# Optimization experiments

Measured on AMD Instinct MI355X. Metric: run time of the kernel, lower is better.

Reference implementation:

```python
import jax, jax.numpy as jnp
import numpy as np

H = 32        # num_attention_heads
KVH = 8       # num_key_value_heads
D = 64        # attention_head_size
WIN = 256     # attention_window_size (left/right)
ROPE_BASE = 10000.0


def setup_inputs() -> dict:
    key = jax.random.key(0)
    k1, k2, k3 = jax.random.split(key, 3)
    B, S = 2, 2048
    return {
        "query_states": jax.random.normal(k1, (B, S, H * D), dtype=jnp.float32),
        "key_states": jax.random.normal(k2, (B, S, KVH * D), dtype=jnp.float32),
        "value_states": jax.random.normal(k3, (B, S, KVH * D), dtype=jnp.float32),
    }


def _rope_cos_sin(seq_len, dtype):
    inv_freq = 1.0 / (ROPE_BASE ** (jnp.arange(0, D, 2, dtype=jnp.float32) / D))  # [D/2]
    pos = jnp.arange(seq_len, dtype=jnp.float32)
    freqs = pos[:, None] * inv_freq[None, :]          # [S, D/2]
    emb = jnp.concatenate([freqs, freqs], axis=-1)    # [S, D]
    return jnp.cos(emb).astype(dtype), jnp.sin(emb).astype(dtype)


def _rotate_half(x):
    x1, x2 = x[..., : D // 2], x[..., D // 2 :]
    return jnp.concatenate([-x2, x1], axis=-1)


def reference(query_states, key_states, value_states):
    B, S, _ = query_states.shape
    n_rep = H // KVH

    q = query_states.reshape(B, S, H, D).transpose(0, 2, 1, 3)        # [B,H,S,D]
    k = key_states.reshape(B, S, KVH, D).transpose(0, 2, 1, 3)        # [B,KVH,S,D]
    v = value_states.reshape(B, S, KVH, D).transpose(0, 2, 1, 3)

    # repeat_kv: [B,KVH,S,D] -> [B,H,S,D]
    k = jnp.repeat(k, n_rep, axis=1)
    v = jnp.repeat(v, n_rep, axis=1)

    cos, sin = _rope_cos_sin(S, q.dtype)   # [S,D]
    cos = cos[None, None]                  # [1,1,S,D]
    sin = sin[None, None]
    q = q * cos + _rotate_half(q) * sin
    k = k * cos + _rotate_half(k) * sin

    scale = 1.0 / jnp.sqrt(jnp.asarray(D, dtype=q.dtype))
    scores = jnp.einsum("bhqd,bhkd->bhqk", q, k) * scale              # [B,H,S,S]

    i = jnp.arange(S)[:, None]
    j = jnp.arange(S)[None, :]
    allowed = (j >= i - WIN) & (j <= i)                               # [S,S]
    scores = jnp.where(allowed[None, None], scores, jnp.finfo(scores.dtype).min)

    probs = jax.nn.softmax(scores, axis=-1)
    out = jnp.einsum("bhqk,bhkd->bhqd", probs, v)                     # [B,H,S,D]
    return out.transpose(0, 2, 1, 3).reshape(B, S, H * D)
```

## Files before the change

kernel.cpp:

```cpp
#include <hip/hip_runtime.h>
#include <math.h>

#define NH   32
#define NKVH 8
#define HD   64
#define WIN  256
#define BB   2
#define SS   2048

typedef short short8 __attribute__((ext_vector_type(8)));
typedef float f32x4  __attribute__((ext_vector_type(4)));

__device__ __forceinline__ ushort f2bf(float x) {
    union { float f; unsigned u; } v; v.f = x;
    unsigned u = v.u + 0x7FFF + ((v.u >> 16) & 1);
    return (ushort)(u >> 16);
}

__device__ __forceinline__ int cvtpk_bf16(float lo, float hi) {
    int r;
    asm("v_cvt_pk_bf16_f32 %0, %1, %2" : "=v"(r) : "v"(lo), "v"(hi));
    return r;
}

__device__ __forceinline__ int swz(int L) { return L ^ (((L >> 7) & 7) << 4); }

__device__ __forceinline__ void stage16(const void* g, void* l) {
    __builtin_amdgcn_global_load_lds(
        (const __attribute__((address_space(1))) unsigned int*)g,
        (__attribute__((address_space(3))) unsigned int*)l, 16, 0, 0);
}

__global__ __launch_bounds__(256) void prep_kv(const float* __restrict__ K,
                                               const float* __restrict__ V,
                                               ushort* __restrict__ Kr,
                                               ushort* __restrict__ Vt) {
    __shared__ __align__(16) ushort ldsK[2048];
    __shared__ __align__(16) ushort ldsV[2048];
    const int bidx = blockIdx.x;
    const int sblk = bidx & 63;
    const int s0   = sblk * 32;
    const int kvh  = (bidx >> 6) & 7;
    const int b    = bidx >> 9;
    const int tid  = threadIdx.x;

    {
        const int key = tid >> 3, dg = tid & 7;
        const int s   = s0 + key;
        const float* krow = K + (size_t)(b * SS + s) * (NKVH * HD) + kvh * HD + dg * 8;
        float x[8];
        *(float4*)(x)     = *(const float4*)(krow);
        *(float4*)(x + 4) = *(const float4*)(krow + 4);
        float inv = __powf(10000.f, -(float)((dg & 3) * 8) * (1.f / 32.f));
        const float ratio = 0.74989420933f;
        ushort out[8];
#pragma unroll
        for (int j = 0; j < 8; ++j) {
            float partner = __shfl(x[j], (tid & 63) ^ 4, 64);
            float sn, cs;
            __sincosf((float)s * inv, &sn, &cs);
            out[j] = f2bf(x[j] * cs + ((dg < 4) ? -partner : partner) * sn);
            inv *= ratio;
        }
        *(short8*)((char*)ldsK + swz(key * 128 + dg * 16)) = *(short8*)out;
    }
    {
        const int kp = tid & 15, dq = tid >> 4;
        const float* v0 = V + (size_t)(b * SS + s0 + 2 * kp) * (NKVH * HD) + kvh * HD + dq * 4;
        float4 a = *(const float4*)v0;
        float4 c = *(const float4*)(v0 + NKVH * HD);
#pragma unroll
        for (int j = 0; j < 4; ++j) {
            int d = dq * 4 + j;
            unsigned w = (unsigned)f2bf(((const float*)&a)[j])
                       | ((unsigned)f2bf(((const float*)&c)[j]) << 16);
            *(unsigned*)((char*)ldsV + swz(d * 64 + kp * 4)) = w;
        }
    }
    __syncthreads();
    char* kc = (char*)(Kr + (size_t)(b * NKVH + kvh) * SS * HD) + (size_t)sblk * 4096;
    char* vc = (char*)(Vt + (size_t)(b * NKVH + kvh) * HD * SS) + (size_t)sblk * 4096;
    *(short8*)(kc + tid * 16) = *(short8*)((char*)ldsK + tid * 16);
    *(short8*)(vc + tid * 16) = *(short8*)((char*)ldsV + tid * 16);
}

__global__ __launch_bounds__(256, 4) void attn_mfma(const float* __restrict__ Q,
                                                    const ushort* __restrict__ Kr,
                                                    const ushort* __restrict__ Vt,
                                                    float* __restrict__ O) {
    __shared__ __align__(16) ushort ldsK[2][2][2048];
    __shared__ __align__(16) ushort ldsV[2][2][2048];
    const int wv = threadIdx.x >> 6, lane = threadIdx.x & 63;
    const int lo16 = lane & 15, quad = lane >> 4;
    const int bidx = (blockIdx.x & 7) * 128 + (blockIdx.x >> 3);
    const int qblk = bidx & 63;
    const int kvh  = (bidx >> 6) & 7;
    const int b    = bidx >> 9;
    const int h    = kvh * 4 + wv;
    const int q0   = qblk * 32;

    float invf[8];
#pragma unroll
    for (int j = 0; j < 8; ++j)
        invf[j] = __powf(10000.f, -(float)(quad * 8 + j) * (1.f / 32.f));

    short8 aq[2][2];
#pragma unroll
    for (int t = 0; t < 2; ++t) {
        int qi = q0 + t * 16 + lo16;
        const float* qrow = Q + (size_t)(b * SS + qi) * (NH * HD) + h * HD;
        float lo[8], hi[8];
        *(float4*)(lo)     = *(const float4*)(qrow + quad * 8);
        *(float4*)(lo + 4) = *(const float4*)(qrow + quad * 8 + 4);
        *(float4*)(hi)     = *(const float4*)(qrow + 32 + quad * 8);
        *(float4*)(hi + 4) = *(const float4*)(qrow + 32 + quad * 8 + 4);
#pragma unroll
        for (int j = 0; j < 8; ++j) {
            float sn, cs;
            __sincosf((float)qi * invf[j], &sn, &cs);
            aq[t][0][j] = (short)f2bf((lo[j] * cs - hi[j] * sn) * 0.125f);
            aq[t][1][j] = (short)f2bf((hi[j] * cs + lo[j] * sn) * 0.125f);
        }
    }

    const char* kbase = (const char*)(Kr + (size_t)(b * NKVH + kvh) * SS * HD);
    const char* vbase = (const char*)(Vt + (size_t)(b * NKVH + kvh) * HD * SS);

    f32x4 acc[2][4];
#pragma unroll
    for (int t = 0; t < 2; ++t)
#pragma unroll
        for (int i = 0; i < 4; ++i) acc[t][i] = (f32x4){0.f, 0.f, 0.f, 0.f};
    float psum[2] = {0.f, 0.f};

    const int idxAB = (lo16 + ((quad & 1) << 5)) << 2;
    const int idxCD = idxAB + 64;
    const bool hiq  = quad >= 2;

    int klo = q0 - WIN; if (klo < 0) klo = 0;
    const int c0  = klo >> 5;
    const int cnt = (q0 >> 5) - c0 + 1;
    const int npairs = (cnt + 1) >> 1;

    auto stagepair = [&](int pidx, int buf) {
        int ca = c0 + 2 * pidx, cb = ca + 1;
        if (ca > SS / 32 - 1) ca = SS / 32 - 1;
        if (cb > SS / 32 - 1) cb = SS / 32 - 1;
        stage16(kbase + (size_t)ca * 4096 + wv * 1024 + lane * 16,
                (char*)&ldsK[buf][0][0] + wv * 1024);
        stage16(vbase + (size_t)ca * 4096 + wv * 1024 + lane * 16,
                (char*)&ldsV[buf][0][0] + wv * 1024);
        stage16(kbase + (size_t)cb * 4096 + wv * 1024 + lane * 16,
                (char*)&ldsK[buf][1][0] + wv * 1024);
        stage16(vbase + (size_t)cb * 4096 + wv * 1024 + lane * 16,
                (char*)&ldsV[buf][1][0] + wv * 1024);
    };

    auto compute = [&](int kb, const char* kl, const char* vl) {
        short8 k0 = *(const short8*)(kl + swz(lo16 * 128 + quad * 16));
        short8 k1 = *(const short8*)(kl + swz(lo16 * 128 + 64 + quad * 16));
        short8 k2 = *(const short8*)(kl + swz((lo16 + 16) * 128 + quad * 16));
        short8 k3 = *(const short8*)(kl + swz((lo16 + 16) * 128 + 64 + quad * 16));

        const f32x4 z = {0.f, 0.f, 0.f, 0.f};
        __builtin_amdgcn_s_setprio(1);
        f32x4 s00 = __builtin_amdgcn_mfma_f32_16x16x32_bf16(k0, aq[0][0], z,   0, 0, 0);
        s00       = __builtin_amdgcn_mfma_f32_16x16x32_bf16(k1, aq[0][1], s00, 0, 0, 0);
        f32x4 s01 = __builtin_amdgcn_mfma_f32_16x16x32_bf16(k2, aq[0][0], z,   0, 0, 0);
        s01       = __builtin_amdgcn_mfma_f32_16x16x32_bf16(k3, aq[0][1], s01, 0, 0, 0);
        f32x4 s10 = __builtin_amdgcn_mfma_f32_16x16x32_bf16(k0, aq[1][0], z,   0, 0, 0);
        s10       = __builtin_amdgcn_mfma_f32_16x16x32_bf16(k1, aq[1][1], s10, 0, 0, 0);
        f32x4 s11 = __builtin_amdgcn_mfma_f32_16x16x32_bf16(k2, aq[1][0], z,   0, 0, 0);
        s11       = __builtin_amdgcn_mfma_f32_16x16x32_bf16(k3, aq[1][1], s11, 0, 0, 0);
        __builtin_amdgcn_s_setprio(0);

        short8 ap[2];
#pragma unroll
        for (int t = 0; t < 2; ++t) {
            const f32x4 sa = t ? s10 : s00;
            const f32x4 sb = t ? s11 : s01;
            const int qtmin = q0 + t * 16;
            const int myq   = qtmin + lo16;
            float p[8];
            if ((kb + 31 > qtmin) || (kb < qtmin + 15 - WIN)) {
#pragma unroll
                for (int r = 0; r < 4; ++r) {
                    int key0 = kb + quad * 4 + r;
                    int key1 = key0 + 16;
                    p[r]     = (key0 <= myq && key0 >= myq - WIN) ? __expf(sa[r]) : 0.f;
                    p[4 + r] = (key1 <= myq && key1 >= myq - WIN) ? __expf(sb[r]) : 0.f;
                }
            } else {
#pragma unroll
                for (int r = 0; r < 4; ++r) { p[r] = __expf(sa[r]); p[4 + r] = __expf(sb[r]); }
            }
            psum[t] += ((p[0] + p[1]) + (p[2] + p[3])) + ((p[4] + p[5]) + (p[6] + p[7]));

            int w0 = cvtpk_bf16(p[0], p[1]);
            int w1 = cvtpk_bf16(p[2], p[3]);
            int w2 = cvtpk_bf16(p[4], p[5]);
            int w3 = cvtpk_bf16(p[6], p[7]);
            int a0 = __builtin_amdgcn_ds_bpermute(idxAB, w0);
            int a2 = __builtin_amdgcn_ds_bpermute(idxAB, w2);
            int b1 = __builtin_amdgcn_ds_bpermute(idxAB, w1);
            int b3 = __builtin_amdgcn_ds_bpermute(idxAB, w3);
            int cc0 = __builtin_amdgcn_ds_bpermute(idxCD, w0);
            int cc2 = __builtin_amdgcn_ds_bpermute(idxCD, w2);
            int d1 = __builtin_amdgcn_ds_bpermute(idxCD, w1);
            int d3 = __builtin_amdgcn_ds_bpermute(idxCD, w3);
            union { int i[4]; short8 s; } u;
            u.i[0] = hiq ? a2  : a0;
            u.i[1] = hiq ? b3  : b1;
            u.i[2] = hiq ? cc2 : cc0;
            u.i[3] = hiq ? d3  : d1;
            ap[t] = u.s;
        }

        short8 vf[4];
#pragma unroll
        for (int i = 0; i < 4; ++i)
            vf[i] = *(const short8*)(vl + swz((i * 16 + lo16) * 64 + quad * 16));

        __builtin_amdgcn_s_setprio(1);
#pragma unroll
        for (int i = 0; i < 4; ++i)
            acc[0][i] = __builtin_amdgcn_mfma_f32_16x16x32_bf16(ap[0], vf[i], acc[0][i], 0, 0, 0);
#pragma unroll
        for (int i = 0; i < 4; ++i)
            acc[1][i] = __builtin_amdgcn_mfma_f32_16x16x32_bf16(ap[1], vf[i], acc[1][i], 0, 0, 0);
        __builtin_amdgcn_s_setprio(0);
    };

    stagepair(0, 0);

    int nb = 0;
    for (int p = 0; p < npairs; ++p, nb ^= 1) {
        stagepair(p + 1, nb ^ 1);
        asm volatile("s_waitcnt vmcnt(4)" ::: "memory");
        __builtin_amdgcn_s_barrier();
        __builtin_amdgcn_sched_barrier(0);
        compute(klo + 2 * p * 32, (const char*)&ldsK[nb][0][0], (const char*)&ldsV[nb][0][0]);
        if (2 * p + 1 < cnt)
            compute(klo + (2 * p + 1) * 32, (const char*)&ldsK[nb][1][0], (const char*)&ldsV[nb][1][0]);
        __builtin_amdgcn_sched_barrier(0);
        __builtin_amdgcn_s_barrier();
    }

#pragma unroll
    for (int t = 0; t < 2; ++t) {
        float ps = psum[t];
        ps += __shfl_xor(ps, 16, 64);
        ps += __shfl_xor(ps, 32, 64);
#pragma unroll
        for (int r = 0; r < 4; ++r) {
            float invr = 1.f / __shfl(ps, quad * 4 + r, 16);
            int qr = q0 + t * 16 + quad * 4 + r;
            size_t orow = ((size_t)(b * SS + qr) * NH + h) * HD;
            O[orow + 0 * 16 + lo16] = acc[t][0][r] * invr;
            O[orow + 1 * 16 + lo16] = acc[t][1][r] * invr;
            O[orow + 2 * 16 + lo16] = acc[t][2][r] * invr;
            O[orow + 3 * 16 + lo16] = acc[t][3][r] * invr;
        }
    }
}

__device__ __forceinline__ float wave_sum(float x) {
#pragma unroll
    for (int off = 32; off > 0; off >>= 1) x += __shfl_xor(x, off, 64);
    return x;
}

__global__ __launch_bounds__(256) void attn_scalar(const float* __restrict__ Q,
                                                   const float* __restrict__ K,
                                                   const float* __restrict__ V,
                                                   float* __restrict__ O) {
    int wave = blockIdx.x * 4 + (threadIdx.x >> 6);
    int lane = threadIdx.x & 63;
    int q  = wave % SS;
    int bh = wave / SS;
    int h  = bh % NH;
    int b  = bh / NH;
    int kvh = h >> 2;

    float inv = __powf(10000.f, -(float)(lane & 31) * (1.f / 32.f));
    float sn, cs;
    __sincosf((float)q * inv, &sn, &cs);

    float qv = Q[(size_t)(b * SS + q) * (NH * HD) + h * HD + lane];
    float qpart = __shfl(qv, lane ^ 32, 64);
    float qrot = (qv * cs + ((lane < 32) ? -qpart : qpart) * sn) * 0.125f;

    const float* vbase = V + (size_t)b * SS * (NKVH * HD) + kvh * HD;
    float m = -1e30f, l = 0.f, acc = 0.f;
    int k0 = q - WIN; if (k0 < 0) k0 = 0;
    for (int k = k0; k <= q; ++k) {
        float kraw = K[(size_t)(b * SS + k) * (NKVH * HD) + kvh * HD + lane];
        float kpart = __shfl(kraw, lane ^ 32, 64);
        float ksn, kcs;
        __sincosf((float)k * inv, &ksn, &kcs);
        float kv = kraw * kcs + ((lane < 32) ? -kpart : kpart) * ksn;
        float vv = vbase[(size_t)k * (NKVH * HD) + lane];
        float score = wave_sum(qrot * kv);
        float mnew  = fmaxf(m, score);
        float alpha = __expf(m - mnew);
        float p     = __expf(score - mnew);
        l   = l * alpha + p;
        acc = acc * alpha + p * vv;
        m   = mnew;
    }
    O[(((size_t)(b * SS + q) * NH) + h) * HD + lane] = acc / l;
}

extern "C" void kernel_launch(void* const* d_in, const int* in_sizes, int n_in,
                              void* d_out, int out_size, void* d_ws, size_t ws_size,
                              hipStream_t stream) {
    const float* Q = (const float*)d_in[0];
    const float* K = (const float*)d_in[1];
    const float* V = (const float*)d_in[2];
    float* O = (float*)d_out;

    size_t kv_elems = (size_t)BB * NKVH * SS * HD;
    size_t need = 2 * kv_elems * sizeof(ushort);

    if (ws_size >= need) {
        ushort* Kr = (ushort*)d_ws;
        ushort* Vt = Kr + kv_elems;
        prep_kv<<<BB * NKVH * (SS / 32), 256, 0, stream>>>(K, V, Kr, Vt);
        attn_mfma<<<BB * NKVH * (SS / 32), 256, 0, stream>>>(Q, Kr, Vt, O);
    } else {
        attn_scalar<<<(BB * NH * SS) / 4, 256, 0, stream>>>(Q, K, V, O);
    }
}
```

Measured before the change: 114.6 us.

## Permute V key order in preprocessing to drop ds_bpermute shuffles of P

The V transpose prep kernel now stores keys in a permuted order that matches the MFMA accumulator layout of the score tile. The attention kernel can then pack exponentiated probabilities straight into the PV MFMA A operand, with no ds_bpermute cross-lane shuffles or selects. This removes eight LDS-path permutes per tile per iteration from the inner loop. The cost is a more complex index mapping in the preprocessing pass, and correctness depends on the permutation matching the MFMA operand layout exactly.

```diff
diff --git a/kernel.cpp b/kernel.cpp
--- a/kernel.cpp
+++ b/kernel.cpp
@@ -66,14 +66,16 @@
     }
     {
         const int kp = tid & 15, dq = tid >> 4;
-        const float* v0 = V + (size_t)(b * SS + s0 + 2 * kp) * (NKVH * HD) + kvh * HD + dq * 4;
+        const int c  = 2 * kp;
+        const int kf = ((c >> 3) * 4) + (c & 3) + (((c >> 2) & 1) * 16);
+        const float* v0 = V + (size_t)(b * SS + s0 + kf) * (NKVH * HD) + kvh * HD + dq * 4;
         float4 a = *(const float4*)v0;
-        float4 c = *(const float4*)(v0 + NKVH * HD);
+        float4 cvec = *(const float4*)(v0 + NKVH * HD);
 #pragma unroll
         for (int j = 0; j < 4; ++j) {
             int d = dq * 4 + j;
             unsigned w = (unsigned)f2bf(((const float*)&a)[j])
-                       | ((unsigned)f2bf(((const float*)&c)[j]) << 16);
+                       | ((unsigned)f2bf(((const float*)&cvec)[j]) << 16);
             *(unsigned*)((char*)ldsV + swz(d * 64 + kp * 4)) = w;
         }
     }
@@ -133,10 +135,6 @@
         for (int i = 0; i < 4; ++i) acc[t][i] = (f32x4){0.f, 0.f, 0.f, 0.f};
     float psum[2] = {0.f, 0.f};
 
-    const int idxAB = (lo16 + ((quad & 1) << 5)) << 2;
-    const int idxCD = idxAB + 64;
-    const bool hiq  = quad >= 2;
-
     int klo = q0 - WIN; if (klo < 0) klo = 0;
     const int c0  = klo >> 5;
     const int cnt = (q0 >> 5) - c0 + 1;
@@ -196,23 +194,11 @@
             }
             psum[t] += ((p[0] + p[1]) + (p[2] + p[3])) + ((p[4] + p[5]) + (p[6] + p[7]));
 
-            int w0 = cvtpk_bf16(p[0], p[1]);
-            int w1 = cvtpk_bf16(p[2], p[3]);
-            int w2 = cvtpk_bf16(p[4], p[5]);
-            int w3 = cvtpk_bf16(p[6], p[7]);
-            int a0 = __builtin_amdgcn_ds_bpermute(idxAB, w0);
-            int a2 = __builtin_amdgcn_ds_bpermute(idxAB, w2);
-            int b1 = __builtin_amdgcn_ds_bpermute(idxAB, w1);
-            int b3 = __builtin_amdgcn_ds_bpermute(idxAB, w3);
-            int cc0 = __builtin_amdgcn_ds_bpermute(idxCD, w0);
-            int cc2 = __builtin_amdgcn_ds_bpermute(idxCD, w2);
-            int d1 = __builtin_amdgcn_ds_bpermute(idxCD, w1);
-            int d3 = __builtin_amdgcn_ds_bpermute(idxCD, w3);
             union { int i[4]; short8 s; } u;
-            u.i[0] = hiq ? a2  : a0;
-            u.i[1] = hiq ? b3  : b1;
-            u.i[2] = hiq ? cc2 : cc0;
-            u.i[3] = hiq ? d3  : d1;
+            u.i[0] = cvtpk_bf16(p[0], p[1]);
+            u.i[1] = cvtpk_bf16(p[2], p[3]);
+            u.i[2] = cvtpk_bf16(p[4], p[5]);
+            u.i[3] = cvtpk_bf16(p[6], p[7]);
             ap[t] = u.s;
         }
 
```

Measured after the change: 113.1 us. No clear change (-1.3%).
